# Optimization experiments

Hardware: AMD Instinct MI355X
Metric: run time of the kernel (lower is better)

The kernel has to match this reference:

```python
import jax, jax.numpy as jnp
import numpy as np

N_NODES = 200000
N_EDGES = 400000
N_GRAPHS = 4096
IN_DIM, HID_DIM, OUT_DIM, EDGE_DIM = 128, 256, 256, 16


def setup_inputs() -> dict:
    key = jax.random.key(0)
    ks = jax.random.split(key, 16)
    x = jax.random.normal(ks[0], (N_NODES, IN_DIM), dtype=jnp.float32)
    edge_attr = jax.random.normal(ks[1], (N_EDGES, EDGE_DIM), dtype=jnp.float32)
    edge_index = jax.random.randint(ks[2], (2, N_EDGES), 0, N_NODES, dtype=jnp.int64)
    batch = jnp.sort(jax.random.randint(ks[3], (N_NODES,), 0, N_GRAPHS, dtype=jnp.int64))

    def lin(k, fan_in, fan_out):
        bound = 1.0 / np.sqrt(fan_in)
        kw, kb = jax.random.split(k)
        W = jax.random.uniform(kw, (fan_in, fan_out), minval=-bound, maxval=bound, dtype=jnp.float32)
        b = jax.random.uniform(kb, (fan_out,), minval=-bound, maxval=bound, dtype=jnp.float32)
        return W, b

    We1, be1 = lin(ks[4], EDGE_DIM, IN_DIM)    # GINEConv1 edge projection
    W1a, b1a = lin(ks[5], IN_DIM, HID_DIM)     # conv1 MLP layer 1
    W1b, b1b = lin(ks[6], HID_DIM, HID_DIM)    # conv1 MLP layer 2
    We2, be2 = lin(ks[7], EDGE_DIM, HID_DIM)   # GINEConv2 edge projection
    W2a, b2a = lin(ks[8], HID_DIM, HID_DIM)    # conv2 MLP layer 1
    W2b, b2b = lin(ks[9], HID_DIM, OUT_DIM)    # conv2 MLP layer 2
    return {"x": x, "edge_attr": edge_attr,
            "We1": We1, "be1": be1, "W1a": W1a, "b1a": b1a, "W1b": W1b, "b1b": b1b,
            "We2": We2, "be2": be2, "W2a": W2a, "b2a": b2a, "W2b": W2b, "b2b": b2b,
            "edge_index": edge_index, "batch": batch}


def _gine_conv(x, edge_attr, src, dst, We, be, Wa, ba, Wb, bb):
    # messages: relu(x_j + lin_edge(e)), scatter-add into destination nodes
    e_proj = edge_attr @ We + be                      # [E, D]
    msg = jax.nn.relu(x[src] + e_proj)                # [E, D]
    aggr = jax.ops.segment_sum(msg, dst, num_segments=x.shape[0])  # [N, D]
    h = x + aggr                                      # (1 + eps) * x_i + aggr, eps=0
    h = jax.nn.relu(h @ Wa + ba)
    return h @ Wb + bb


def reference(x, edge_attr, We1, be1, W1a, b1a, W1b, b1b,
              We2, be2, W2a, b2a, W2b, b2b, edge_index, batch):
    src, dst = edge_index[0], edge_index[1]
    h = jax.nn.relu(_gine_conv(x, edge_attr, src, dst, We1, be1, W1a, b1a, W1b, b1b))
    h = jax.nn.relu(_gine_conv(h, edge_attr, src, dst, We2, be2, W2a, b2a, W2b, b2b))
    # global mean pool over graphs
    sums = jax.ops.segment_sum(h, batch, num_segments=N_GRAPHS)            # [G, D]
    counts = jax.ops.segment_sum(jnp.ones((h.shape[0],), h.dtype), batch,
                                 num_segments=N_GRAPHS)                    # [G]
    return sums / jnp.maximum(counts, 1.0)[:, None]
```

## Files before the change

### kernel.cpp

```cpp
#include <hip/hip_runtime.h>
#include <hip/hip_bf16.h>

typedef float f32x4 __attribute__((ext_vector_type(4)));
typedef float f32x2 __attribute__((ext_vector_type(2)));
typedef unsigned short u16x2 __attribute__((ext_vector_type(2)));
typedef unsigned short u16x4 __attribute__((ext_vector_type(4)));
typedef unsigned short u16x8 __attribute__((ext_vector_type(8)));
typedef short s16x8 __attribute__((ext_vector_type(8)));

#define NN 200000
#define NE 400000
#define NG 4096
#define SCHUNK 1024
#define NSCAN ((NN + SCHUNK - 1) / SCHUNK)

template<int C> struct VecT;
template<> struct VecT<2> { using T = u16x2; };
template<> struct VecT<4> { using T = u16x4; };

__device__ __forceinline__ unsigned short f2bf(float f) {
    union { float f; unsigned int u; } v; v.f = f;
    unsigned int r = v.u + 0x7FFF + ((v.u >> 16) & 1);
    return (unsigned short)(r >> 16);
}
__device__ __forceinline__ float bf2f(unsigned short b) {
    union { unsigned int u; float f; } v; v.u = ((unsigned int)b) << 16;
    return v.f;
}

__global__ void detect_i64(const int* __restrict__ ei, int* __restrict__ flag) {
    unsigned long long m = __ballot(ei[threadIdx.x * 2 + 1] == 0);
    if (threadIdx.x == 0) *flag = (~m == 0ULL) ? 1 : 0;
}
__device__ __forceinline__ int load_idx(const int* p, long long i, int f64) {
    return f64 ? (int)((const long long*)p)[i] : p[i];
}

__global__ void wt_conv(const float* __restrict__ W, unsigned short* __restrict__ Wt,
                        int K, int N) {
    int tid = blockIdx.x * 256 + threadIdx.x;
    if (tid >= K * N) return;
    int n = tid / K, k = tid - n * K;
    Wt[tid] = f2bf(W[(size_t)k * N + n]);
}

__global__ __launch_bounds__(256) void copy_int(const int* __restrict__ a,
                                                int* __restrict__ b, int n) {
    int i = blockIdx.x * 256 + threadIdx.x;
    if (i < n) b[i] = a[i];
}

__global__ __launch_bounds__(256) void x2bf(const float* __restrict__ x,
                                            unsigned short* __restrict__ xh) {
    long long i = ((long long)blockIdx.x * 256 + threadIdx.x) * 4;
    if (i >= (long long)NN * 128) return;
    f32x4 v = *(const f32x4*)(x + i);
    u16x4 o; o.x = f2bf(v.x); o.y = f2bf(v.y); o.z = f2bf(v.z); o.w = f2bf(v.w);
    *(u16x4*)(xh + i) = o;
}

__global__ __launch_bounds__(256) void ea_perm(const float* __restrict__ ea,
                                               const int* __restrict__ eidx,
                                               const int* __restrict__ totE_p,
                                               float* __restrict__ eac) {
    int j = blockIdx.x * 256 + threadIdx.x;
    if (j >= *totE_p) return;
    int e = eidx[j];
    if ((unsigned)e >= NE) e = 0;
    const float* s = ea + (size_t)e * 16;
    float* d = eac + (size_t)j * 16;
#pragma unroll
    for (int k = 0; k < 4; ++k)
        *(f32x4*)(d + k * 4) = *(const f32x4*)(s + k * 4);
}

__global__ __launch_bounds__(256) void hist_dst(const int* __restrict__ ei,
                                                const int* __restrict__ flag,
                                                int* __restrict__ deg) {
    int e = blockIdx.x * 256 + threadIdx.x;
    if (e >= NE) return;
    int f64 = *flag;
    int s = load_idx(ei, e, f64);
    int d = load_idx(ei, (long long)NE + e, f64);
    if ((unsigned)s < NN && (unsigned)d < NN) atomicAdd(&deg[d], 1);
}

__global__ __launch_bounds__(256) void scan_bsum(const int* __restrict__ deg,
                                                 int* __restrict__ bsum) {
    __shared__ int red[256];
    int t = threadIdx.x, base = blockIdx.x * SCHUNK + t * 4;
    int s = 0;
#pragma unroll
    for (int c = 0; c < 4; ++c) { int i = base + c; if (i < NN) s += deg[i]; }
    red[t] = s; __syncthreads();
    for (int o = 128; o > 0; o >>= 1) { if (t < o) red[t] += red[t + o]; __syncthreads(); }
    if (t == 0) bsum[blockIdx.x] = red[0];
}

__global__ void scan_carry(int* __restrict__ bsum, int* __restrict__ rowptr_end) {
    if (threadIdx.x == 0) {
        int run = 0;
        for (int i = 0; i < NSCAN; ++i) { int v = bsum[i]; bsum[i] = run; run += v; }
        *rowptr_end = run;
    }
}

__global__ __launch_bounds__(256) void scan_final(const int* __restrict__ deg,
                                                  const int* __restrict__ bsum,
                                                  int* __restrict__ rowptr) {
    __shared__ int lds[256];
    int t = threadIdx.x, base = blockIdx.x * SCHUNK + t * 4;
    int v[4], s = 0;
#pragma unroll
    for (int c = 0; c < 4; ++c) { int i = base + c; v[c] = (i < NN) ? deg[i] : 0; s += v[c]; }
    lds[t] = s; __syncthreads();
    for (int o = 1; o < 256; o <<= 1) {
        int x = 0;
        if (t >= o) x = lds[t - o];
        __syncthreads();
        if (t >= o) lds[t] += x;
        __syncthreads();
    }
    int run = lds[t] - s + bsum[blockIdx.x];
#pragma unroll
    for (int c = 0; c < 4; ++c) { int i = base + c; if (i < NN) rowptr[i] = run; run += v[c]; }
}

__global__ __launch_bounds__(256) void fill_csr(const int* __restrict__ ei,
                                                const int* __restrict__ flag,
                                                int* __restrict__ cursor,
                                                int* __restrict__ srcs,
                                                int* __restrict__ eidx) {
    int e = blockIdx.x * 256 + threadIdx.x;
    if (e >= NE) return;
    int f64 = *flag;
    int s = load_idx(ei, e, f64);
    int d = load_idx(ei, (long long)NE + e, f64);
    if ((unsigned)s >= NN || (unsigned)d >= NN) return;
    int pos = atomicAdd(&cursor[d], 1);
    if ((unsigned)pos < NE) { srcs[pos] = s; eidx[pos] = e; }
}

template<int C>
__global__ __launch_bounds__(256)
void msg_build(const unsigned short* __restrict__ xh,
               const float* __restrict__ eac,
               const float* __restrict__ We, const float* __restrict__ be,
               const int* __restrict__ srcs, const int* __restrict__ totE_p,
               unsigned short* __restrict__ M) {
    using XV = typename VecT<C>::T;
    constexpr int D = 64 * C;
    constexpr int C2 = C / 2;
    const int wid  = (blockIdx.x * 256 + threadIdx.x) >> 6;
    const int lane = threadIdx.x & 63;
    const int totE = *totE_p;
    const int col = lane * C;

    f32x2 w2[16][C2], bb2[C2];
#pragma unroll
    for (int k = 0; k < 16; ++k)
#pragma unroll
        for (int c = 0; c < C2; ++c)
            w2[k][c] = *(const f32x2*)(We + k * D + col + 2 * c);
#pragma unroll
    for (int c = 0; c < C2; ++c) bb2[c] = *(const f32x2*)(be + col + 2 * c);

    const int j0 = wid * 4;
    int sv[4];
    XV xv[4];
#pragma unroll
    for (int u = 0; u < 4; ++u) {
        int j = j0 + u;
        sv[u] = (j < totE) ? srcs[j] : -1;
    }
#pragma unroll
    for (int u = 0; u < 4; ++u) {
        if ((unsigned)sv[u] < NN)
            xv[u] = *(const XV*)(xh + (size_t)sv[u] * D + col);
        else
            xv[u] = (XV)0;
    }
#pragma unroll
    for (int u = 0; u < 4; ++u) {
        int j = j0 + u;
        if (j >= totE) continue;
        const float* eap = eac + (size_t)j * 16;
        f32x4 e0 = *(const f32x4*)eap;
        f32x4 e1 = *(const f32x4*)(eap + 4);
        f32x4 e2 = *(const f32x4*)(eap + 8);
        f32x4 e3 = *(const f32x4*)(eap + 12);
        f32x2 m2[C2];
#pragma unroll
        for (int c = 0; c < C2; ++c) {
            f32x2 xx; xx.x = bf2f(xv[u][2 * c]); xx.y = bf2f(xv[u][2 * c + 1]);
            m2[c] = bb2[c] + xx;
        }
#pragma unroll
        for (int k = 0; k < 4; ++k) {
            f32x2 k0; k0.x = e0[k]; k0.y = e0[k];
            f32x2 k1; k1.x = e1[k]; k1.y = e1[k];
            f32x2 k2; k2.x = e2[k]; k2.y = e2[k];
            f32x2 k3; k3.x = e3[k]; k3.y = e3[k];
#pragma unroll
            for (int c = 0; c < C2; ++c) {
                m2[c] += k0 * w2[k][c];
                m2[c] += k1 * w2[4 + k][c];
                m2[c] += k2 * w2[8 + k][c];
                m2[c] += k3 * w2[12 + k][c];
            }
        }
        XV o;
#pragma unroll
        for (int c = 0; c < C2; ++c) {
            o[2 * c]     = f2bf(fmaxf(m2[c].x, 0.f));
            o[2 * c + 1] = f2bf(fmaxf(m2[c].y, 0.f));
        }
        *(XV*)(M + (size_t)j * D + col) = o;
    }
}

template<int C>
__global__ __launch_bounds__(256)
void seg_sum(const unsigned short* __restrict__ M, const int* __restrict__ rowptr,
             const unsigned short* __restrict__ self, unsigned short* __restrict__ outp) {
    using XV = typename VecT<C>::T;
    constexpr int D = 64 * C;
    const int node = (blockIdx.x * 256 + threadIdx.x) >> 6;
    const int lane = threadIdx.x & 63;
    if (node >= NN) return;
    const int col = lane * C;
    int lo = rowptr[node], hi = rowptr[node + 1];
    if (lo > hi || (unsigned)hi > NE) { lo = 0; hi = 0; }

    float a[C];
    XV sv = *(const XV*)(self + (size_t)node * D + col);
#pragma unroll
    for (int c = 0; c < C; ++c) a[c] = bf2f(sv[c]);

    int j = lo;
    for (; j + 1 < hi; j += 2) {
        XV m0 = *(const XV*)(M + (size_t)j * D + col);
        XV m1 = *(const XV*)(M + (size_t)(j + 1) * D + col);
#pragma unroll
        for (int c = 0; c < C; ++c) a[c] += bf2f(m0[c]) + bf2f(m1[c]);
    }
    if (j < hi) {
        XV m0 = *(const XV*)(M + (size_t)j * D + col);
#pragma unroll
        for (int c = 0; c < C; ++c) a[c] += bf2f(m0[c]);
    }
    XV o;
#pragma unroll
    for (int c = 0; c < C; ++c) o[c] = f2bf(a[c]);
    *(XV*)(outp + (size_t)node * D + col) = o;
}

template<int K, typename CT>
__global__ __launch_bounds__(256)
void gemm_bias_relu(const unsigned short* __restrict__ A,
                    const unsigned short* __restrict__ Wt, const float* __restrict__ bias,
                    CT* __restrict__ C) {
    constexpr int LDT = 68;
    __shared__ unsigned short As[64 * LDT];
    __shared__ unsigned short Bs[256 * LDT];
    const int m0 = blockIdx.x * 64;
    const int tid = threadIdx.x;
    const int wave = tid >> 6;
    const int lane = tid & 63;
    const int lm = lane & 15;
    const int lq = lane >> 4;
    const int nw = wave * 64;

    const int srow = tid >> 2;
    const int scol = (tid & 3) * 16;

    f32x4 acc[4][4] = {};

    for (int k0 = 0; k0 < K; k0 += 64) {
        {
            const unsigned short* src = A + (size_t)(m0 + srow) * K + k0 + scol;
            unsigned short* dst = As + srow * LDT + scol;
            *(u16x8*)(dst)     = *(const u16x8*)(src);
            *(u16x8*)(dst + 8) = *(const u16x8*)(src + 8);
        }
#pragma unroll
        for (int rr = 0; rr < 4; ++rr) {
            int r = srow + rr * 64;
            const unsigned short* src = Wt + (size_t)r * K + k0 + scol;
            unsigned short* dst = Bs + r * LDT + scol;
            *(u16x8*)(dst)     = *(const u16x8*)(src);
            *(u16x8*)(dst + 8) = *(const u16x8*)(src + 8);
        }
        __syncthreads();
#pragma unroll
        for (int ks = 0; ks < 2; ++ks) {
            s16x8 af[4], bf[4];
#pragma unroll
            for (int mt = 0; mt < 4; ++mt)
                af[mt] = *(const s16x8*)(As + (mt * 16 + lm) * LDT + ks * 32 + lq * 8);
#pragma unroll
            for (int nt = 0; nt < 4; ++nt)
                bf[nt] = *(const s16x8*)(Bs + (nw + nt * 16 + lm) * LDT + ks * 32 + lq * 8);
#pragma unroll
            for (int mt = 0; mt < 4; ++mt)
#pragma unroll
                for (int nt = 0; nt < 4; ++nt)
                    acc[mt][nt] = __builtin_amdgcn_mfma_f32_16x16x32_bf16(
                        af[mt], bf[nt], acc[mt][nt], 0, 0, 0);
        }
        __syncthreads();
    }

#pragma unroll
    for (int mt = 0; mt < 4; ++mt) {
        const int row = m0 + mt * 16 + lq * 4;
#pragma unroll
        for (int nt = 0; nt < 4; ++nt) {
            int col = nw + nt * 16 + lm;
            float bv = bias[col];
#pragma unroll
            for (int r = 0; r < 4; ++r) {
                float v = fmaxf(acc[mt][nt][r] + bv, 0.f);
                if constexpr (sizeof(CT) == 2)
                    C[(size_t)(row + r) * 256 + col] = (CT)f2bf(v);
                else
                    C[(size_t)(row + r) * 256 + col] = (CT)v;
            }
        }
    }
}

__global__ __launch_bounds__(256)
void pool_mean(const float* __restrict__ h, const int* __restrict__ batch,
               const int* __restrict__ flag, float* __restrict__ out) {
    const int f64 = *flag;
    int g = blockIdx.x;
    int a = 0, b = NN;
    while (a < b) { int m = (a + b) >> 1; if (load_idx(batch, m, f64) < g) a = m + 1; else b = m; }
    int lo = a;
    b = NN;
    while (a < b) { int m = (a + b) >> 1; if (load_idx(batch, m, f64) < g + 1) a = m + 1; else b = m; }
    int hi = a;
    int f = threadIdx.x;
    float s = 0.f;
    for (int n = lo; n < hi; ++n) s += h[(size_t)n * 256 + f];
    float cnt = (float)(hi - lo);
    out[(size_t)g * 256 + f] = s / fmaxf(cnt, 1.f);
}

extern "C" void kernel_launch(void* const* d_in, const int* in_sizes, int n_in,
                              void* d_out, int out_size, void* d_ws, size_t ws_size,
                              hipStream_t stream) {
    const float* x   = (const float*)d_in[0];
    const float* ea  = (const float*)d_in[1];
    const float* We1 = (const float*)d_in[2];
    const float* be1 = (const float*)d_in[3];
    const float* W1a = (const float*)d_in[4];
    const float* b1a = (const float*)d_in[5];
    const float* W1b = (const float*)d_in[6];
    const float* b1b = (const float*)d_in[7];
    const float* We2 = (const float*)d_in[8];
    const float* be2 = (const float*)d_in[9];
    const float* W2a = (const float*)d_in[10];
    const float* b2a = (const float*)d_in[11];
    const float* W2b = (const float*)d_in[12];
    const float* b2b = (const float*)d_in[13];
    const int*   ei  = (const int*)d_in[14];
    const int*   bat = (const int*)d_in[15];
    float* out = (float*)d_out;

    char* ws = (char*)d_ws;
    const size_t SZH = (size_t)NN * 256 * 2;
    unsigned short* A  = (unsigned short*)ws;
    unsigned short* B  = (unsigned short*)(ws + SZH);
    unsigned short* Cr = (unsigned short*)(ws + 2 * SZH);
    char* Dr = ws + 3 * SZH;
    char* q = Dr;
    int* deg    = (int*)q; q += (size_t)NN * 4;
    int* rowptr = (int*)q; q += (size_t)(NN + 1) * 4;
    int* cursor = (int*)q; q += (size_t)NN * 4;
    int* srcs   = (int*)q; q += (size_t)NE * 4;
    int* eidx   = (int*)q; q += (size_t)NE * 4;
    int* bsum   = (int*)q; q += (size_t)NSCAN * 4;
    q = Dr + ((q - Dr + 63) & ~63ll);
    float*          eac = (float*)q; q += (size_t)NE * 16 * 4;
    unsigned short* xh  = (unsigned short*)q;
    char* p = ws + 4 * SZH;
    unsigned short* Wt1a = (unsigned short*)p; p += 128 * 256 * 2;
    unsigned short* Wt1b = (unsigned short*)p; p += 256 * 256 * 2;
    unsigned short* Wt2a = (unsigned short*)p; p += 256 * 256 * 2;
    unsigned short* Wt2b = (unsigned short*)p; p += 256 * 256 * 2;
    int* flag = (int*)p;

    detect_i64<<<1, 64, 0, stream>>>(ei, flag);
    wt_conv<<<(128 * 256 + 255) / 256, 256, 0, stream>>>(W1a, Wt1a, 128, 256);
    wt_conv<<<(256 * 256 + 255) / 256, 256, 0, stream>>>(W1b, Wt1b, 256, 256);
    wt_conv<<<(256 * 256 + 255) / 256, 256, 0, stream>>>(W2a, Wt2a, 256, 256);
    wt_conv<<<(256 * 256 + 255) / 256, 256, 0, stream>>>(W2b, Wt2b, 256, 256);

    hipMemsetAsync(deg, 0, (size_t)NN * 4, stream);
    hist_dst<<<(NE + 255) / 256, 256, 0, stream>>>(ei, flag, deg);
    scan_bsum<<<NSCAN, 256, 0, stream>>>(deg, bsum);
    scan_carry<<<1, 64, 0, stream>>>(bsum, rowptr + NN);
    scan_final<<<NSCAN, 256, 0, stream>>>(deg, bsum, rowptr);
    copy_int<<<(NN + 255) / 256, 256, 0, stream>>>(rowptr, cursor, NN);
    fill_csr<<<(NE + 255) / 256, 256, 0, stream>>>(ei, flag, cursor, srcs, eidx);
    ea_perm<<<(NE + 255) / 256, 256, 0, stream>>>(ea, eidx, rowptr + NN, eac);
    x2bf<<<(NN * 128 / 4 + 255) / 256, 256, 0, stream>>>(x, xh);

    const int GM_BLK = NE / 16;
    const int GS_BLK = NN / 4;
    const int GG_BLK = NN / 64;

    msg_build<2><<<GM_BLK, 256, 0, stream>>>(xh, eac, We1, be1, srcs, rowptr + NN, A);
    seg_sum<2><<<GS_BLK, 256, 0, stream>>>(A, rowptr, xh, B);
    gemm_bias_relu<128, unsigned short><<<GG_BLK, 256, 0, stream>>>(B, Wt1a, b1a, Cr);
    gemm_bias_relu<256, unsigned short><<<GG_BLK, 256, 0, stream>>>(Cr, Wt1b, b1b, A);

    msg_build<4><<<GM_BLK, 256, 0, stream>>>(A, eac, We2, be2, srcs, rowptr + NN, B);
    seg_sum<4><<<GS_BLK, 256, 0, stream>>>(B, rowptr, A, A);
    gemm_bias_relu<256, unsigned short><<<GG_BLK, 256, 0, stream>>>(A, Wt2a, b2a, B);
    gemm_bias_relu<256, float><<<GG_BLK, 256, 0, stream>>>(B, Wt2b, b2b, (float*)Cr);

    pool_mean<<<NG, 256, 0, stream>>>((const float*)Cr, bat, flag, out);
}
```

Baseline: 1.035 ms.

## Fuse edge message construction into CSR segment-sum aggregation kernel

```diff
diff --git a/kernel.cpp b/kernel.cpp
--- a/kernel.cpp
+++ b/kernel.cpp
@@ -142,116 +142,96 @@
 }
 
 template<int C>
+__device__ __forceinline__ void edge_acc(const f32x2 (&w2)[16][C / 2],
+                                         const f32x2 (&bb2)[C / 2],
+                                         const float* __restrict__ eap,
+                                         typename VecT<C>::T xv,
+                                         f32x2 (&a2)[C / 2]) {
+    constexpr int C2 = C / 2;
+    f32x4 e0 = *(const f32x4*)eap;
+    f32x4 e1 = *(const f32x4*)(eap + 4);
+    f32x4 e2 = *(const f32x4*)(eap + 8);
+    f32x4 e3 = *(const f32x4*)(eap + 12);
+    f32x2 m2[C2];
+#pragma unroll
+    for (int c = 0; c < C2; ++c) {
+        f32x2 xx; xx.x = bf2f(xv[2 * c]); xx.y = bf2f(xv[2 * c + 1]);
+        m2[c] = bb2[c] + xx;
+    }
+#pragma unroll
+    for (int k = 0; k < 4; ++k) {
+        f32x2 k0; k0.x = e0[k]; k0.y = e0[k];
+        f32x2 k1; k1.x = e1[k]; k1.y = e1[k];
+        f32x2 k2; k2.x = e2[k]; k2.y = e2[k];
+        f32x2 k3; k3.x = e3[k]; k3.y = e3[k];
+#pragma unroll
+        for (int c = 0; c < C2; ++c) {
+            m2[c] += k0 * w2[k][c];
+            m2[c] += k1 * w2[4 + k][c];
+            m2[c] += k2 * w2[8 + k][c];
+            m2[c] += k3 * w2[12 + k][c];
+        }
+    }
+#pragma unroll
+    for (int c = 0; c < C2; ++c) {
+        a2[c].x += fmaxf(m2[c].x, 0.f);
+        a2[c].y += fmaxf(m2[c].y, 0.f);
+    }
+}
+
+template<int C>
 __global__ __launch_bounds__(256)
-void msg_build(const unsigned short* __restrict__ xh,
+void gine_aggr(const unsigned short* __restrict__ xh,
+               const unsigned short* __restrict__ self,
                const float* __restrict__ eac,
                const float* __restrict__ We, const float* __restrict__ be,
-               const int* __restrict__ srcs, const int* __restrict__ totE_p,
-               unsigned short* __restrict__ M) {
+               const int* __restrict__ srcs, const int* __restrict__ rowptr,
+               unsigned short* __restrict__ outp) {
     using XV = typename VecT<C>::T;
     constexpr int D = 64 * C;
     constexpr int C2 = C / 2;
-    const int wid  = (blockIdx.x * 256 + threadIdx.x) >> 6;
-    const int lane = threadIdx.x & 63;
-    const int totE = *totE_p;
-    const int col = lane * C;
-
-    f32x2 w2[16][C2], bb2[C2];
-#pragma unroll
-    for (int k = 0; k < 16; ++k)
-#pragma unroll
-        for (int c = 0; c < C2; ++c)
-            w2[k][c] = *(const f32x2*)(We + k * D + col + 2 * c);
-#pragma unroll
-    for (int c = 0; c < C2; ++c) bb2[c] = *(const f32x2*)(be + col + 2 * c);
-
-    const int j0 = wid * 4;
-    int sv[4];
-    XV xv[4];
-#pragma unroll
-    for (int u = 0; u < 4; ++u) {
-        int j = j0 + u;
-        sv[u] = (j < totE) ? srcs[j] : -1;
-    }
-#pragma unroll
-    for (int u = 0; u < 4; ++u) {
-        if ((unsigned)sv[u] < NN)
-            xv[u] = *(const XV*)(xh + (size_t)sv[u] * D + col);
-        else
-            xv[u] = (XV)0;
-    }
-#pragma unroll
-    for (int u = 0; u < 4; ++u) {
-        int j = j0 + u;
-        if (j >= totE) continue;
-        const float* eap = eac + (size_t)j * 16;
-        f32x4 e0 = *(const f32x4*)eap;
-        f32x4 e1 = *(const f32x4*)(eap + 4);
-        f32x4 e2 = *(const f32x4*)(eap + 8);
-        f32x4 e3 = *(const f32x4*)(eap + 12);
-        f32x2 m2[C2];
-#pragma unroll
-        for (int c = 0; c < C2; ++c) {
-            f32x2 xx; xx.x = bf2f(xv[u][2 * c]); xx.y = bf2f(xv[u][2 * c + 1]);
-            m2[c] = bb2[c] + xx;
-        }
-#pragma unroll
-        for (int k = 0; k < 4; ++k) {
-            f32x2 k0; k0.x = e0[k]; k0.y = e0[k];
-            f32x2 k1; k1.x = e1[k]; k1.y = e1[k];
-            f32x2 k2; k2.x = e2[k]; k2.y = e2[k];
-            f32x2 k3; k3.x = e3[k]; k3.y = e3[k];
-#pragma unroll
-            for (int c = 0; c < C2; ++c) {
-                m2[c] += k0 * w2[k][c];
-                m2[c] += k1 * w2[4 + k][c];
-                m2[c] += k2 * w2[8 + k][c];
-                m2[c] += k3 * w2[12 + k][c];
-            }
-        }
-        XV o;
-#pragma unroll
-        for (int c = 0; c < C2; ++c) {
-            o[2 * c]     = f2bf(fmaxf(m2[c].x, 0.f));
-            o[2 * c + 1] = f2bf(fmaxf(m2[c].y, 0.f));
-        }
-        *(XV*)(M + (size_t)j * D + col) = o;
-    }
-}
-
-template<int C>
-__global__ __launch_bounds__(256)
-void seg_sum(const unsigned short* __restrict__ M, const int* __restrict__ rowptr,
-             const unsigned short* __restrict__ self, unsigned short* __restrict__ outp) {
-    using XV = typename VecT<C>::T;
-    constexpr int D = 64 * C;
     const int node = (blockIdx.x * 256 + threadIdx.x) >> 6;
     const int lane = threadIdx.x & 63;
     if (node >= NN) return;
     const int col = lane * C;
+
     int lo = rowptr[node], hi = rowptr[node + 1];
     if (lo > hi || (unsigned)hi > NE) { lo = 0; hi = 0; }
 
-    float a[C];
     XV sv = *(const XV*)(self + (size_t)node * D + col);
-#pragma unroll
-    for (int c = 0; c < C; ++c) a[c] = bf2f(sv[c]);
+
+    f32x2 w2[16][C2], bb2[C2];
+#pragma unroll
+    for (int k = 0; k < 16; ++k)
+#pragma unroll
+        for (int c = 0; c < C2; ++c)
+            w2[k][c] = *(const f32x2*)(We + k * D + col + 2 * c);
+#pragma unroll
+    for (int c = 0; c < C2; ++c) bb2[c] = *(const f32x2*)(be + col + 2 * c);
+
+    f32x2 a2[C2];
+#pragma unroll
+    for (int c = 0; c < C2; ++c) { a2[c].x = bf2f(sv[2 * c]); a2[c].y = bf2f(sv[2 * c + 1]); }
 
     int j = lo;
     for (; j + 1 < hi; j += 2) {
-        XV m0 = *(const XV*)(M + (size_t)j * D + col);
-        XV m1 = *(const XV*)(M + (size_t)(j + 1) * D + col);
-#pragma unroll
-        for (int c = 0; c < C; ++c) a[c] += bf2f(m0[c]) + bf2f(m1[c]);
+        int s0 = srcs[j], s1 = srcs[j + 1];
+        XV x0 = (XV)0, x1 = (XV)0;
+        if ((unsigned)s0 < NN) x0 = *(const XV*)(xh + (size_t)s0 * D + col);
+        if ((unsigned)s1 < NN) x1 = *(const XV*)(xh + (size_t)s1 * D + col);
+        edge_acc<C>(w2, bb2, eac + (size_t)j * 16, x0, a2);
+        edge_acc<C>(w2, bb2, eac + (size_t)(j + 1) * 16, x1, a2);
     }
     if (j < hi) {
-        XV m0 = *(const XV*)(M + (size_t)j * D + col);
-#pragma unroll
-        for (int c = 0; c < C; ++c) a[c] += bf2f(m0[c]);
-    }
+        int s0 = srcs[j];
+        XV x0 = (XV)0;
+        if ((unsigned)s0 < NN) x0 = *(const XV*)(xh + (size_t)s0 * D + col);
+        edge_acc<C>(w2, bb2, eac + (size_t)j * 16, x0, a2);
+    }
+
     XV o;
 #pragma unroll
-    for (int c = 0; c < C; ++c) o[c] = f2bf(a[c]);
+    for (int c = 0; c < C2; ++c) { o[2 * c] = f2bf(a2[c].x); o[2 * c + 1] = f2bf(a2[c].y); }
     *(XV*)(outp + (size_t)node * D + col) = o;
 }
 
@@ -408,19 +388,16 @@
     ea_perm<<<(NE + 255) / 256, 256, 0, stream>>>(ea, eidx, rowptr + NN, eac);
     x2bf<<<(NN * 128 / 4 + 255) / 256, 256, 0, stream>>>(x, xh);
 
-    const int GM_BLK = NE / 16;
     const int GS_BLK = NN / 4;
     const int GG_BLK = NN / 64;
 
-    msg_build<2><<<GM_BLK, 256, 0, stream>>>(xh, eac, We1, be1, srcs, rowptr + NN, A);
-    seg_sum<2><<<GS_BLK, 256, 0, stream>>>(A, rowptr, xh, B);
+    gine_aggr<2><<<GS_BLK, 256, 0, stream>>>(xh, xh, eac, We1, be1, srcs, rowptr, B);
     gemm_bias_relu<128, unsigned short><<<GG_BLK, 256, 0, stream>>>(B, Wt1a, b1a, Cr);
     gemm_bias_relu<256, unsigned short><<<GG_BLK, 256, 0, stream>>>(Cr, Wt1b, b1b, A);
 
-    msg_build<4><<<GM_BLK, 256, 0, stream>>>(A, eac, We2, be2, srcs, rowptr + NN, B);
-    seg_sum<4><<<GS_BLK, 256, 0, stream>>>(B, rowptr, A, A);
-    gemm_bias_relu<256, unsigned short><<<GG_BLK, 256, 0, stream>>>(A, Wt2a, b2a, B);
-    gemm_bias_relu<256, float><<<GG_BLK, 256, 0, stream>>>(B, Wt2b, b2b, (float*)Cr);
+    gine_aggr<4><<<GS_BLK, 256, 0, stream>>>(A, A, eac, We2, be2, srcs, rowptr, B);
+    gemm_bias_relu<256, unsigned short><<<GG_BLK, 256, 0, stream>>>(B, Wt2a, b2a, A);
+    gemm_bias_relu<256, float><<<GG_BLK, 256, 0, stream>>>(A, Wt2b, b2b, (float*)Cr);
 
     pool_mean<<<NG, 256, 0, stream>>>((const float*)Cr, bat, flag, out);
 }
```

New measurement: 1.088 ms. 5.1% more time.

## Fuse message build and segment sum into per-node-block LDS accumulation kernel

Applied to the files above, without the earlier changes.

```diff
diff --git a/kernel.cpp b/kernel.cpp
--- a/kernel.cpp
+++ b/kernel.cpp
@@ -130,6 +130,7 @@
                                                 const int* __restrict__ flag,
                                                 int* __restrict__ cursor,
                                                 int* __restrict__ srcs,
+                                                int* __restrict__ dsts,
                                                 int* __restrict__ eidx) {
     int e = blockIdx.x * 256 + threadIdx.x;
     if (e >= NE) return;
@@ -138,22 +139,26 @@
     int d = load_idx(ei, (long long)NE + e, f64);
     if ((unsigned)s >= NN || (unsigned)d >= NN) return;
     int pos = atomicAdd(&cursor[d], 1);
-    if ((unsigned)pos < NE) { srcs[pos] = s; eidx[pos] = e; }
-}
-
-template<int C>
+    if ((unsigned)pos < NE) { srcs[pos] = s; dsts[pos] = d; eidx[pos] = e; }
+}
+
+template<int C, int NB>
 __global__ __launch_bounds__(256)
-void msg_build(const unsigned short* __restrict__ xh,
-               const float* __restrict__ eac,
-               const float* __restrict__ We, const float* __restrict__ be,
-               const int* __restrict__ srcs, const int* __restrict__ totE_p,
-               unsigned short* __restrict__ M) {
+void gine_blk(const unsigned short* __restrict__ xh,
+              const unsigned short* __restrict__ self,
+              const float* __restrict__ eac,
+              const float* __restrict__ We, const float* __restrict__ be,
+              const int* __restrict__ srcs, const int* __restrict__ dsts,
+              const int* __restrict__ rowptr,
+              unsigned short* __restrict__ outp) {
     using XV = typename VecT<C>::T;
     constexpr int D = 64 * C;
     constexpr int C2 = C / 2;
-    const int wid  = (blockIdx.x * 256 + threadIdx.x) >> 6;
-    const int lane = threadIdx.x & 63;
-    const int totE = *totE_p;
+    __shared__ float acc[NB * D];
+    const int n0 = blockIdx.x * NB;
+    const int tid = threadIdx.x;
+    const int lane = tid & 63;
+    const int wave = tid >> 6;
     const int col = lane * C;
 
     f32x2 w2[16][C2], bb2[C2];
@@ -165,94 +170,81 @@
 #pragma unroll
     for (int c = 0; c < C2; ++c) bb2[c] = *(const f32x2*)(be + col + 2 * c);
 
-    const int j0 = wid * 4;
-    int sv[4];
-    XV xv[4];
-#pragma unroll
-    for (int u = 0; u < 4; ++u) {
-        int j = j0 + u;
-        sv[u] = (j < totE) ? srcs[j] : -1;
-    }
-#pragma unroll
-    for (int u = 0; u < 4; ++u) {
-        if ((unsigned)sv[u] < NN)
-            xv[u] = *(const XV*)(xh + (size_t)sv[u] * D + col);
-        else
-            xv[u] = (XV)0;
-    }
-#pragma unroll
-    for (int u = 0; u < 4; ++u) {
-        int j = j0 + u;
-        if (j >= totE) continue;
-        const float* eap = eac + (size_t)j * 16;
-        f32x4 e0 = *(const f32x4*)eap;
-        f32x4 e1 = *(const f32x4*)(eap + 4);
-        f32x4 e2 = *(const f32x4*)(eap + 8);
-        f32x4 e3 = *(const f32x4*)(eap + 12);
-        f32x2 m2[C2];
-#pragma unroll
-        for (int c = 0; c < C2; ++c) {
-            f32x2 xx; xx.x = bf2f(xv[u][2 * c]); xx.y = bf2f(xv[u][2 * c + 1]);
-            m2[c] = bb2[c] + xx;
-        }
-#pragma unroll
-        for (int k = 0; k < 4; ++k) {
-            f32x2 k0; k0.x = e0[k]; k0.y = e0[k];
-            f32x2 k1; k1.x = e1[k]; k1.y = e1[k];
-            f32x2 k2; k2.x = e2[k]; k2.y = e2[k];
-            f32x2 k3; k3.x = e3[k]; k3.y = e3[k];
+    for (int r = wave; r < NB; r += 4) {
+        XV sv = *(const XV*)(self + (size_t)(n0 + r) * D + col);
+        float* ap = acc + r * D + col;
+#pragma unroll
+        for (int c = 0; c < C; ++c) ap[c] = bf2f(sv[c]);
+    }
+
+    int lo = rowptr[n0], hi = rowptr[n0 + NB];
+    if (lo < 0 || hi < lo || hi > NE) { lo = 0; hi = 0; }
+    __syncthreads();
+
+    for (int j0 = lo + wave * 4; j0 < hi; j0 += 16) {
+        int sv[4], dv[4];
+        XV xv[4];
+#pragma unroll
+        for (int u = 0; u < 4; ++u) {
+            int j = j0 + u;
+            sv[u] = (j < hi) ? srcs[j] : -1;
+            dv[u] = (j < hi) ? (dsts[j] - n0) : -1;
+        }
+#pragma unroll
+        for (int u = 0; u < 4; ++u) {
+            if ((unsigned)sv[u] < NN)
+                xv[u] = *(const XV*)(xh + (size_t)sv[u] * D + col);
+            else
+                xv[u] = (XV)0;
+        }
+#pragma unroll
+        for (int u = 0; u < 4; ++u) {
+            int j = j0 + u;
+            if (j >= hi) continue;
+            const float* eap = eac + (size_t)j * 16;
+            f32x4 e0 = *(const f32x4*)eap;
+            f32x4 e1 = *(const f32x4*)(eap + 4);
+            f32x4 e2 = *(const f32x4*)(eap + 8);
+            f32x4 e3 = *(const f32x4*)(eap + 12);
+            f32x2 m2[C2];
 #pragma unroll
             for (int c = 0; c < C2; ++c) {
-                m2[c] += k0 * w2[k][c];
-                m2[c] += k1 * w2[4 + k][c];
-                m2[c] += k2 * w2[8 + k][c];
-                m2[c] += k3 * w2[12 + k][c];
+                f32x2 xx; xx.x = bf2f(xv[u][2 * c]); xx.y = bf2f(xv[u][2 * c + 1]);
+                m2[c] = bb2[c] + xx;
             }
-        }
+#pragma unroll
+            for (int k = 0; k < 4; ++k) {
+                f32x2 k0; k0.x = e0[k]; k0.y = e0[k];
+                f32x2 k1; k1.x = e1[k]; k1.y = e1[k];
+                f32x2 k2; k2.x = e2[k]; k2.y = e2[k];
+                f32x2 k3; k3.x = e3[k]; k3.y = e3[k];
+#pragma unroll
+                for (int c = 0; c < C2; ++c) {
+                    m2[c] += k0 * w2[k][c];
+                    m2[c] += k1 * w2[4 + k][c];
+                    m2[c] += k2 * w2[8 + k][c];
+                    m2[c] += k3 * w2[12 + k][c];
+                }
+            }
+            if ((unsigned)dv[u] < NB) {
+                float* ap = acc + dv[u] * D + col;
+#pragma unroll
+                for (int c = 0; c < C2; ++c) {
+                    atomicAdd(ap + 2 * c,     fmaxf(m2[c].x, 0.f));
+                    atomicAdd(ap + 2 * c + 1, fmaxf(m2[c].y, 0.f));
+                }
+            }
+        }
+    }
+    __syncthreads();
+
+    for (int r = wave; r < NB; r += 4) {
+        const float* ap = acc + r * D + col;
         XV o;
 #pragma unroll
-        for (int c = 0; c < C2; ++c) {
-            o[2 * c]     = f2bf(fmaxf(m2[c].x, 0.f));
-            o[2 * c + 1] = f2bf(fmaxf(m2[c].y, 0.f));
-        }
-        *(XV*)(M + (size_t)j * D + col) = o;
-    }
-}
-
-template<int C>
-__global__ __launch_bounds__(256)
-void seg_sum(const unsigned short* __restrict__ M, const int* __restrict__ rowptr,
-             const unsigned short* __restrict__ self, unsigned short* __restrict__ outp) {
-    using XV = typename VecT<C>::T;
-    constexpr int D = 64 * C;
-    const int node = (blockIdx.x * 256 + threadIdx.x) >> 6;
-    const int lane = threadIdx.x & 63;
-    if (node >= NN) return;
-    const int col = lane * C;
-    int lo = rowptr[node], hi = rowptr[node + 1];
-    if (lo > hi || (unsigned)hi > NE) { lo = 0; hi = 0; }
-
-    float a[C];
-    XV sv = *(const XV*)(self + (size_t)node * D + col);
-#pragma unroll
-    for (int c = 0; c < C; ++c) a[c] = bf2f(sv[c]);
-
-    int j = lo;
-    for (; j + 1 < hi; j += 2) {
-        XV m0 = *(const XV*)(M + (size_t)j * D + col);
-        XV m1 = *(const XV*)(M + (size_t)(j + 1) * D + col);
-#pragma unroll
-        for (int c = 0; c < C; ++c) a[c] += bf2f(m0[c]) + bf2f(m1[c]);
-    }
-    if (j < hi) {
-        XV m0 = *(const XV*)(M + (size_t)j * D + col);
-#pragma unroll
-        for (int c = 0; c < C; ++c) a[c] += bf2f(m0[c]);
-    }
-    XV o;
-#pragma unroll
-    for (int c = 0; c < C; ++c) o[c] = f2bf(a[c]);
-    *(XV*)(outp + (size_t)node * D + col) = o;
+        for (int c = 0; c < C; ++c) o[c] = f2bf(ap[c]);
+        *(XV*)(outp + (size_t)(n0 + r) * D + col) = o;
+    }
 }
 
 template<int K, typename CT>
@@ -380,6 +372,7 @@
     int* rowptr = (int*)q; q += (size_t)(NN + 1) * 4;
     int* cursor = (int*)q; q += (size_t)NN * 4;
     int* srcs   = (int*)q; q += (size_t)NE * 4;
+    int* dsts   = (int*)q; q += (size_t)NE * 4;
     int* eidx   = (int*)q; q += (size_t)NE * 4;
     int* bsum   = (int*)q; q += (size_t)NSCAN * 4;
     q = Dr + ((q - Dr + 63) & ~63ll);
@@ -404,23 +397,20 @@
     scan_carry<<<1, 64, 0, stream>>>(bsum, rowptr + NN);
     scan_final<<<NSCAN, 256, 0, stream>>>(deg, bsum, rowptr);
     copy_int<<<(NN + 255) / 256, 256, 0, stream>>>(rowptr, cursor, NN);
-    fill_csr<<<(NE + 255) / 256, 256, 0, stream>>>(ei, flag, cursor, srcs, eidx);
+    fill_csr<<<(NE + 255) / 256, 256, 0, stream>>>(ei, flag, cursor, srcs, dsts, eidx);
     ea_perm<<<(NE + 255) / 256, 256, 0, stream>>>(ea, eidx, rowptr + NN, eac);
     x2bf<<<(NN * 128 / 4 + 255) / 256, 256, 0, stream>>>(x, xh);
 
-    const int GM_BLK = NE / 16;
-    const int GS_BLK = NN / 4;
+    const int GB_BLK = NN / 32;
     const int GG_BLK = NN / 64;
 
-    msg_build<2><<<GM_BLK, 256, 0, stream>>>(xh, eac, We1, be1, srcs, rowptr + NN, A);
-    seg_sum<2><<<GS_BLK, 256, 0, stream>>>(A, rowptr, xh, B);
+    gine_blk<2, 32><<<GB_BLK, 256, 0, stream>>>(xh, xh, eac, We1, be1, srcs, dsts, rowptr, B);
     gemm_bias_relu<128, unsigned short><<<GG_BLK, 256, 0, stream>>>(B, Wt1a, b1a, Cr);
     gemm_bias_relu<256, unsigned short><<<GG_BLK, 256, 0, stream>>>(Cr, Wt1b, b1b, A);
 
-    msg_build<4><<<GM_BLK, 256, 0, stream>>>(A, eac, We2, be2, srcs, rowptr + NN, B);
-    seg_sum<4><<<GS_BLK, 256, 0, stream>>>(B, rowptr, A, A);
-    gemm_bias_relu<256, unsigned short><<<GG_BLK, 256, 0, stream>>>(A, Wt2a, b2a, B);
-    gemm_bias_relu<256, float><<<GG_BLK, 256, 0, stream>>>(B, Wt2b, b2b, (float*)Cr);
+    gine_blk<4, 32><<<GB_BLK, 256, 0, stream>>>(A, A, eac, We2, be2, srcs, dsts, rowptr, B);
+    gemm_bias_relu<256, unsigned short><<<GG_BLK, 256, 0, stream>>>(B, Wt2a, b2a, A);
+    gemm_bias_relu<256, float><<<GG_BLK, 256, 0, stream>>>(A, Wt2b, b2b, (float*)Cr);
 
     pool_mean<<<NG, 256, 0, stream>>>((const float*)Cr, bat, flag, out);
 }
```

Result: slower. 1.481 ms (+43.1%).

## Fuse both MLP GEMMs per layer, merge cursor copy into scan, unroll msg_build

Applied to the files above, without the earlier changes.

```diff
diff --git a/kernel.cpp b/kernel.cpp
--- a/kernel.cpp
+++ b/kernel.cpp
@@ -42,12 +42,6 @@
     if (tid >= K * N) return;
     int n = tid / K, k = tid - n * K;
     Wt[tid] = f2bf(W[(size_t)k * N + n]);
-}
-
-__global__ __launch_bounds__(256) void copy_int(const int* __restrict__ a,
-                                                int* __restrict__ b, int n) {
-    int i = blockIdx.x * 256 + threadIdx.x;
-    if (i < n) b[i] = a[i];
 }
 
 __global__ __launch_bounds__(256) void x2bf(const float* __restrict__ x,
@@ -107,7 +101,8 @@
 
 __global__ __launch_bounds__(256) void scan_final(const int* __restrict__ deg,
                                                   const int* __restrict__ bsum,
-                                                  int* __restrict__ rowptr) {
+                                                  int* __restrict__ rowptr,
+                                                  int* __restrict__ cursor) {
     __shared__ int lds[256];
     int t = threadIdx.x, base = blockIdx.x * SCHUNK + t * 4;
     int v[4], s = 0;
@@ -123,7 +118,11 @@
     }
     int run = lds[t] - s + bsum[blockIdx.x];
 #pragma unroll
-    for (int c = 0; c < 4; ++c) { int i = base + c; if (i < NN) rowptr[i] = run; run += v[c]; }
+    for (int c = 0; c < 4; ++c) {
+        int i = base + c;
+        if (i < NN) { rowptr[i] = run; cursor[i] = run; }
+        run += v[c];
+    }
 }
 
 __global__ __launch_bounds__(256) void fill_csr(const int* __restrict__ ei,
@@ -141,7 +140,7 @@
     if ((unsigned)pos < NE) { srcs[pos] = s; eidx[pos] = e; }
 }
 
-template<int C>
+template<int C, int U>
 __global__ __launch_bounds__(256)
 void msg_build(const unsigned short* __restrict__ xh,
                const float* __restrict__ eac,
@@ -165,23 +164,23 @@
 #pragma unroll
     for (int c = 0; c < C2; ++c) bb2[c] = *(const f32x2*)(be + col + 2 * c);
 
-    const int j0 = wid * 4;
-    int sv[4];
-    XV xv[4];
-#pragma unroll
-    for (int u = 0; u < 4; ++u) {
+    const int j0 = wid * U;
+    int sv[U];
+    XV xv[U];
+#pragma unroll
+    for (int u = 0; u < U; ++u) {
         int j = j0 + u;
         sv[u] = (j < totE) ? srcs[j] : -1;
     }
 #pragma unroll
-    for (int u = 0; u < 4; ++u) {
+    for (int u = 0; u < U; ++u) {
         if ((unsigned)sv[u] < NN)
             xv[u] = *(const XV*)(xh + (size_t)sv[u] * D + col);
         else
             xv[u] = (XV)0;
     }
 #pragma unroll
-    for (int u = 0; u < 4; ++u) {
+    for (int u = 0; u < U; ++u) {
         int j = j0 + u;
         if (j >= totE) continue;
         const float* eap = eac + (size_t)j * 16;
@@ -255,14 +254,17 @@
     *(XV*)(outp + (size_t)node * D + col) = o;
 }
 
-template<int K, typename CT>
+template<int K1, typename CT>
 __global__ __launch_bounds__(256)
-void gemm_bias_relu(const unsigned short* __restrict__ A,
-                    const unsigned short* __restrict__ Wt, const float* __restrict__ bias,
-                    CT* __restrict__ C) {
+void gemm2_fused(const unsigned short* __restrict__ A,
+                 const unsigned short* __restrict__ Wta, const float* __restrict__ ba,
+                 const unsigned short* __restrict__ Wtb, const float* __restrict__ bb,
+                 CT* __restrict__ C) {
     constexpr int LDT = 68;
+    constexpr int LDM = 260;
     __shared__ unsigned short As[64 * LDT];
     __shared__ unsigned short Bs[256 * LDT];
+    __shared__ unsigned short Ms[64 * LDM];
     const int m0 = blockIdx.x * 64;
     const int tid = threadIdx.x;
     const int wave = tid >> 6;
@@ -274,57 +276,104 @@
     const int srow = tid >> 2;
     const int scol = (tid & 3) * 16;
 
-    f32x4 acc[4][4] = {};
-
-    for (int k0 = 0; k0 < K; k0 += 64) {
-        {
-            const unsigned short* src = A + (size_t)(m0 + srow) * K + k0 + scol;
-            unsigned short* dst = As + srow * LDT + scol;
-            *(u16x8*)(dst)     = *(const u16x8*)(src);
-            *(u16x8*)(dst + 8) = *(const u16x8*)(src + 8);
-        }
-#pragma unroll
-        for (int rr = 0; rr < 4; ++rr) {
-            int r = srow + rr * 64;
-            const unsigned short* src = Wt + (size_t)r * K + k0 + scol;
-            unsigned short* dst = Bs + r * LDT + scol;
-            *(u16x8*)(dst)     = *(const u16x8*)(src);
-            *(u16x8*)(dst + 8) = *(const u16x8*)(src + 8);
-        }
-        __syncthreads();
-#pragma unroll
-        for (int ks = 0; ks < 2; ++ks) {
-            s16x8 af[4], bf[4];
-#pragma unroll
-            for (int mt = 0; mt < 4; ++mt)
-                af[mt] = *(const s16x8*)(As + (mt * 16 + lm) * LDT + ks * 32 + lq * 8);
-#pragma unroll
-            for (int nt = 0; nt < 4; ++nt)
-                bf[nt] = *(const s16x8*)(Bs + (nw + nt * 16 + lm) * LDT + ks * 32 + lq * 8);
-#pragma unroll
-            for (int mt = 0; mt < 4; ++mt)
+    {
+        f32x4 acc[4][4] = {};
+        for (int k0 = 0; k0 < K1; k0 += 64) {
+            {
+                const unsigned short* src = A + (size_t)(m0 + srow) * K1 + k0 + scol;
+                unsigned short* dst = As + srow * LDT + scol;
+                *(u16x8*)(dst)     = *(const u16x8*)(src);
+                *(u16x8*)(dst + 8) = *(const u16x8*)(src + 8);
+            }
+#pragma unroll
+            for (int rr = 0; rr < 4; ++rr) {
+                int r = srow + rr * 64;
+                const unsigned short* src = Wta + (size_t)r * K1 + k0 + scol;
+                unsigned short* dst = Bs + r * LDT + scol;
+                *(u16x8*)(dst)     = *(const u16x8*)(src);
+                *(u16x8*)(dst + 8) = *(const u16x8*)(src + 8);
+            }
+            __syncthreads();
+#pragma unroll
+            for (int ks = 0; ks < 2; ++ks) {
+                s16x8 af[4], bf[4];
+#pragma unroll
+                for (int mt = 0; mt < 4; ++mt)
+                    af[mt] = *(const s16x8*)(As + (mt * 16 + lm) * LDT + ks * 32 + lq * 8);
 #pragma unroll
                 for (int nt = 0; nt < 4; ++nt)
-                    acc[mt][nt] = __builtin_amdgcn_mfma_f32_16x16x32_bf16(
-                        af[mt], bf[nt], acc[mt][nt], 0, 0, 0);
-        }
-        __syncthreads();
-    }
-
-#pragma unroll
-    for (int mt = 0; mt < 4; ++mt) {
-        const int row = m0 + mt * 16 + lq * 4;
-#pragma unroll
-        for (int nt = 0; nt < 4; ++nt) {
-            int col = nw + nt * 16 + lm;
-            float bv = bias[col];
-#pragma unroll
-            for (int r = 0; r < 4; ++r) {
-                float v = fmaxf(acc[mt][nt][r] + bv, 0.f);
-                if constexpr (sizeof(CT) == 2)
-                    C[(size_t)(row + r) * 256 + col] = (CT)f2bf(v);
-                else
-                    C[(size_t)(row + r) * 256 + col] = (CT)v;
+                    bf[nt] = *(const s16x8*)(Bs + (nw + nt * 16 + lm) * LDT + ks * 32 + lq * 8);
+#pragma unroll
+                for (int mt = 0; mt < 4; ++mt)
+#pragma unroll
+                    for (int nt = 0; nt < 4; ++nt)
+                        acc[mt][nt] = __builtin_amdgcn_mfma_f32_16x16x32_bf16(
+                            af[mt], bf[nt], acc[mt][nt], 0, 0, 0);
+            }
+            __syncthreads();
+        }
+#pragma unroll
+        for (int mt = 0; mt < 4; ++mt) {
+            const int row = mt * 16 + lq * 4;
+#pragma unroll
+            for (int nt = 0; nt < 4; ++nt) {
+                int coln = nw + nt * 16 + lm;
+                float bv = ba[coln];
+#pragma unroll
+                for (int r = 0; r < 4; ++r) {
+                    float v = fmaxf(acc[mt][nt][r] + bv, 0.f);
+                    Ms[(row + r) * LDM + coln] = f2bf(v);
+                }
+            }
+        }
+    }
+    __syncthreads();
+
+    {
+        f32x4 acc[4][4] = {};
+        for (int k0 = 0; k0 < 256; k0 += 64) {
+#pragma unroll
+            for (int rr = 0; rr < 4; ++rr) {
+                int r = srow + rr * 64;
+                const unsigned short* src = Wtb + (size_t)r * 256 + k0 + scol;
+                unsigned short* dst = Bs + r * LDT + scol;
+                *(u16x8*)(dst)     = *(const u16x8*)(src);
+                *(u16x8*)(dst + 8) = *(const u16x8*)(src + 8);
+            }
+            __syncthreads();
+#pragma unroll
+            for (int ks = 0; ks < 2; ++ks) {
+                s16x8 af[4], bf[4];
+#pragma unroll
+                for (int mt = 0; mt < 4; ++mt)
+                    af[mt] = *(const s16x8*)(Ms + (mt * 16 + lm) * LDM + k0 + ks * 32 + lq * 8);
+#pragma unroll
+                for (int nt = 0; nt < 4; ++nt)
+                    bf[nt] = *(const s16x8*)(Bs + (nw + nt * 16 + lm) * LDT + ks * 32 + lq * 8);
+#pragma unroll
+                for (int mt = 0; mt < 4; ++mt)
+#pragma unroll
+                    for (int nt = 0; nt < 4; ++nt)
+                        acc[mt][nt] = __builtin_amdgcn_mfma_f32_16x16x32_bf16(
+                            af[mt], bf[nt], acc[mt][nt], 0, 0, 0);
+            }
+            __syncthreads();
+        }
+#pragma unroll
+        for (int mt = 0; mt < 4; ++mt) {
+            const int row = m0 + mt * 16 + lq * 4;
+#pragma unroll
+            for (int nt = 0; nt < 4; ++nt) {
+                int coln = nw + nt * 16 + lm;
+                float bv = bb[coln];
+#pragma unroll
+                for (int r = 0; r < 4; ++r) {
+                    float v = fmaxf(acc[mt][nt][r] + bv, 0.f);
+                    if constexpr (sizeof(CT) == 2)
+                        C[(size_t)(row + r) * 256 + coln] = (CT)f2bf(v);
+                    else
+                        C[(size_t)(row + r) * 256 + coln] = (CT)v;
+                }
             }
         }
     }
@@ -402,25 +451,22 @@
     hist_dst<<<(NE + 255) / 256, 256, 0, stream>>>(ei, flag, deg);
     scan_bsum<<<NSCAN, 256, 0, stream>>>(deg, bsum);
     scan_carry<<<1, 64, 0, stream>>>(bsum, rowptr + NN);
-    scan_final<<<NSCAN, 256, 0, stream>>>(deg, bsum, rowptr);
-    copy_int<<<(NN + 255) / 256, 256, 0, stream>>>(rowptr, cursor, NN);
+    scan_final<<<NSCAN, 256, 0, stream>>>(deg, bsum, rowptr, cursor);
     fill_csr<<<(NE + 255) / 256, 256, 0, stream>>>(ei, flag, cursor, srcs, eidx);
     ea_perm<<<(NE + 255) / 256, 256, 0, stream>>>(ea, eidx, rowptr + NN, eac);
     x2bf<<<(NN * 128 / 4 + 255) / 256, 256, 0, stream>>>(x, xh);
 
-    const int GM_BLK = NE / 16;
+    const int GM_BLK = NE / 32;
     const int GS_BLK = NN / 4;
     const int GG_BLK = NN / 64;
 
-    msg_build<2><<<GM_BLK, 256, 0, stream>>>(xh, eac, We1, be1, srcs, rowptr + NN, A);
+    msg_build<2, 8><<<GM_BLK, 256, 0, stream>>>(xh, eac, We1, be1, srcs, rowptr + NN, A);
     seg_sum<2><<<GS_BLK, 256, 0, stream>>>(A, rowptr, xh, B);
-    gemm_bias_relu<128, unsigned short><<<GG_BLK, 256, 0, stream>>>(B, Wt1a, b1a, Cr);
-    gemm_bias_relu<256, unsigned short><<<GG_BLK, 256, 0, stream>>>(Cr, Wt1b, b1b, A);
-
-    msg_build<4><<<GM_BLK, 256, 0, stream>>>(A, eac, We2, be2, srcs, rowptr + NN, B);
+    gemm2_fused<128, unsigned short><<<GG_BLK, 256, 0, stream>>>(B, Wt1a, b1a, Wt1b, b1b, A);
+
+    msg_build<4, 8><<<GM_BLK, 256, 0, stream>>>(A, eac, We2, be2, srcs, rowptr + NN, B);
     seg_sum<4><<<GS_BLK, 256, 0, stream>>>(B, rowptr, A, A);
-    gemm_bias_relu<256, unsigned short><<<GG_BLK, 256, 0, stream>>>(A, Wt2a, b2a, B);
-    gemm_bias_relu<256, float><<<GG_BLK, 256, 0, stream>>>(B, Wt2b, b2b, (float*)Cr);
+    gemm2_fused<256, float><<<GG_BLK, 256, 0, stream>>>(A, Wt2a, b2a, Wt2b, b2b, (float*)Cr);
 
     pool_mean<<<NG, 256, 0, stream>>>((const float*)Cr, bat, flag, out);
 }
```

Result: faster. 934.2 us (-9.7%).
